# Optimization experiments

Hardware: AMD Instinct MI355X
Metric: run time of the kernel (lower is better)

Reference implementation:

```python
import jax, jax.numpy as jnp
import numpy as np

B, N, D = 256, 131072, 256
TEMP = 0.05
EPS_SM = 1e-6
EPS_LOG = 1e-6
NUM_CLUSTERS = 1000


def _l2norm(x):
    return x / jnp.linalg.norm(x, axis=-1, keepdims=True)


def setup_inputs() -> dict:
    key = jax.random.key(0)
    k1, k2, k3, k4, k5 = jax.random.split(key, 5)
    # re-ID features are L2-normalized in practice; keeps exp(logits/temp) finite
    inputs = _l2norm(jax.random.normal(k1, (B, D), jnp.float32))
    indexes = jax.random.randint(k2, (B,), 0, N)
    labels = jax.random.randint(k3, (N,), 0, NUM_CLUSTERS)  # pseudo cluster ids buffer
    cluster_features = _l2norm(jax.random.normal(k4, (N, D), jnp.float32))
    instance_features = _l2norm(jax.random.normal(k5, (N, D), jnp.float32))
    return {
        "inputs": inputs,
        "cluster_features": cluster_features,
        "instance_features": instance_features,
        "indexes": indexes,
        "labels": labels,
    }


def reference(inputs, cluster_features, instance_features, indexes, labels):
    # targets = labels[indexes]
    targets = labels[indexes]
    # bank similarity GEMM, temperature scaling
    logits = jnp.matmul(inputs, cluster_features.T) / TEMP  # [B, N]
    # module's custom softmax: exp / (sum + eps)  (intentionally no max-subtract)
    exps = jnp.exp(logits)
    masked_sim = exps / (jnp.sum(exps, axis=1, keepdims=True) + EPS_SM)
    logp = jnp.log(masked_sim + EPS_LOG)
    # F.nll_loss: mean of -logp at target column
    loss = -jnp.mean(jnp.take_along_axis(logp, targets[:, None], axis=1))
    return loss
```

## Files before the change

### kernel.cpp

```cpp
#include <hip/hip_runtime.h>
#include <hip/hip_bf16.h>
#include <cstdint>

#define B_ 256
#define N_ 131072
#define D_ 256
#define INV_TEMP 20.0f
#define EPS_SM 1e-6f
#define EPS_LOG 1e-6f

#define TPB 512
#define BROWS 256
#define BN 32
#define BK 64
#define NCHUNK 32
#define LDB 72
#define BUFE (BN * LDB)
#define NSLOT 32
#define NBLK (N_ / BROWS)

typedef __bf16 bf16_t;
typedef bf16_t bf16x8 __attribute__((ext_vector_type(8)));
typedef float f32x4 __attribute__((ext_vector_type(4)));

__device__ inline ushort f2bf(float f) {
  uint32_t u = __builtin_bit_cast(uint32_t, f);
  u += 0x7FFFu + ((u >> 16) & 1u);
  return (ushort)(u >> 16);
}

__global__ __launch_bounds__(TPB, 4)
void gemm_rowsum_fused(const float* __restrict__ inp, const float* __restrict__ cf,
                       const int* __restrict__ idx, const int* __restrict__ lab,
                       float* __restrict__ rowsum, unsigned* __restrict__ counter,
                       float* __restrict__ out) {
  __shared__ ushort smem[B_ * LDB];
  __shared__ unsigned done;
  const int tid  = threadIdx.x;
  const int wave = tid >> 6;
  const int lane = tid & 63;
  const int m15  = lane & 15;
  const int q    = lane >> 4;

  const size_t nbase = (size_t)blockIdx.x * BROWS;
  const int brow = tid >> 4, bcg = tid & 15;
#define LDADDR(c) (cf + (nbase + (size_t)((c) >> 2) * BN + brow) * D_ + ((c) & 3) * BK + bcg * 4)

  float4 ldbuf[2];
  ldbuf[0] = *(const float4*)LDADDR(0);
  ldbuf[1] = *(const float4*)LDADDR(1);

  bf16x8 areg[8][2];
#pragma unroll
  for (int kc = 0; kc < 4; ++kc) {
    const int row = tid >> 1, half = tid & 1;
    const float* src = inp + row * D_ + kc * BK + half * 32;
#pragma unroll
    for (int i = 0; i < 8; ++i) {
      const float4 v = *(const float4*)(src + i * 4);
      ushort4 w = {f2bf(v.x), f2bf(v.y), f2bf(v.z), f2bf(v.w)};
      *(ushort4*)(&smem[row * LDB + half * 32 + i * 4]) = w;
    }
    __syncthreads();
#pragma unroll
    for (int mb = 0; mb < 2; ++mb)
#pragma unroll
      for (int ks = 0; ks < 2; ++ks)
        areg[kc * 2 + ks][mb] = __builtin_bit_cast(
            bf16x8, *(const uint4*)(&smem[(wave * 32 + mb * 16 + m15) * LDB + ks * 32 + q * 8]));
    __syncthreads();
  }

  f32x4 acc[2][2];
  float rs[2][4];
#pragma unroll
  for (int mb = 0; mb < 2; ++mb) {
#pragma unroll
    for (int nb = 0; nb < 2; ++nb) acc[mb][nb] = (f32x4){0.f, 0.f, 0.f, 0.f};
#pragma unroll
    for (int r = 0; r < 4; ++r) rs[mb][r] = 0.f;
  }

  {
    const float4 v = ldbuf[0];
    ushort4 w = {f2bf(v.x), f2bf(v.y), f2bf(v.z), f2bf(v.w)};
    *(ushort4*)(&smem[brow * LDB + bcg * 4]) = w;
  }
  ldbuf[0] = *(const float4*)LDADDR(2);

#pragma unroll
  for (int c = 0; c < NCHUNK; ++c) {
    __syncthreads();
    const ushort* bs = &smem[(c & 1) * BUFE];
#pragma unroll
    for (int ks = 0; ks < 2; ++ks) {
      bf16x8 bfr[2];
#pragma unroll
      for (int nb = 0; nb < 2; ++nb)
        bfr[nb] = __builtin_bit_cast(
            bf16x8, *(const uint4*)(&bs[(nb * 16 + m15) * LDB + ks * 32 + q * 8]));
#pragma unroll
      for (int mb = 0; mb < 2; ++mb)
#pragma unroll
        for (int nb = 0; nb < 2; ++nb)
          acc[mb][nb] = __builtin_amdgcn_mfma_f32_16x16x32_bf16(
              areg[(c & 3) * 2 + ks][mb], bfr[nb], acc[mb][nb], 0, 0, 0);
    }
    if ((c & 3) == 3) {
#pragma unroll
      for (int mb = 0; mb < 2; ++mb)
#pragma unroll
        for (int nb = 0; nb < 2; ++nb)
#pragma unroll
          for (int r = 0; r < 4; ++r)
            rs[mb][r] += __expf(acc[mb][nb][r] * INV_TEMP);
      if (c + 1 < NCHUNK) {
#pragma unroll
        for (int mb = 0; mb < 2; ++mb)
#pragma unroll
          for (int nb = 0; nb < 2; ++nb) acc[mb][nb] = (f32x4){0.f, 0.f, 0.f, 0.f};
      }
    }
    if (c + 1 < NCHUNK) {
      const float4 v = ldbuf[(c + 1) & 1];
      ushort4 w = {f2bf(v.x), f2bf(v.y), f2bf(v.z), f2bf(v.w)};
      *(ushort4*)(&smem[((c + 1) & 1) * BUFE + brow * LDB + bcg * 4]) = w;
    }
    if (c + 3 < NCHUNK) {
      ldbuf[(c + 1) & 1] = *(const float4*)LDADDR(c + 3);
    }
  }

#pragma unroll
  for (int off = 8; off >= 1; off >>= 1)
#pragma unroll
    for (int mb = 0; mb < 2; ++mb)
#pragma unroll
      for (int r = 0; r < 4; ++r)
        rs[mb][r] += __shfl_xor(rs[mb][r], off, 64);

  if (m15 == 0) {
    float* slot = rowsum + (blockIdx.x & (NSLOT - 1)) * B_;
#pragma unroll
    for (int mb = 0; mb < 2; ++mb)
#pragma unroll
      for (int r = 0; r < 4; ++r)
        atomicAdd(&slot[wave * 32 + mb * 16 + q * 4 + r], rs[mb][r]);
  }
#undef LDADDR

  __syncthreads();
  if (tid == 0) {
    __threadfence();
    const unsigned prev = __hip_atomic_fetch_add(counter, 1u, __ATOMIC_ACQ_REL,
                                                 __HIP_MEMORY_SCOPE_AGENT);
    done = (prev == (unsigned)(NBLK - 1)) ? 1u : 0u;
  }
  __syncthreads();
  if (done) {
    __threadfence();
    float* red = (float*)smem;
    const int b = tid >> 1, part = tid & 1;
    const int t = lab[idx[b]];
    const float4* a4 = (const float4*)(inp + b * D_ + part * 128);
    const float4* c4 = (const float4*)(cf + (size_t)t * D_ + part * 128);
    float dot = 0.f;
#pragma unroll
    for (int i = 0; i < 32; ++i) {
      const float4 x = a4[i], y = c4[i];
      dot += x.x * y.x + x.y * y.y + x.z * y.z + x.w * y.w;
    }
    red[tid] = dot;
    __syncthreads();
    if (tid < 256) {
      const float d = red[2 * tid] + red[2 * tid + 1];
      float S = 0.f;
#pragma unroll
      for (int s = 0; s < NSLOT; ++s)
        S += __hip_atomic_load(&rowsum[s * B_ + tid], __ATOMIC_RELAXED,
                               __HIP_MEMORY_SCOPE_AGENT);
      red[512 + tid] = __logf(__expf(d * INV_TEMP) / (S + EPS_SM) + EPS_LOG);
    }
    __syncthreads();
    for (int off = 128; off >= 1; off >>= 1) {
      if (tid < off) red[512 + tid] += red[512 + tid + off];
      __syncthreads();
    }
    if (tid == 0) out[0] = -red[512] * (1.0f / 256.0f);
  }
}

extern "C" void kernel_launch(void* const* d_in, const int* in_sizes, int n_in,
                              void* d_out, int out_size, void* d_ws, size_t ws_size,
                              hipStream_t stream) {
  const float* inp = (const float*)d_in[0];
  const float* cf  = (const float*)d_in[1];
  const int* idx = (const int*)d_in[3];
  const int* lab = (const int*)d_in[4];
  float* out = (float*)d_out;
  float* rowsum = (float*)d_ws;
  unsigned* counter = (unsigned*)(rowsum + NSLOT * B_);

  hipMemsetAsync(d_ws, 0, (NSLOT * B_ + 16) * sizeof(float), stream);
  gemm_rowsum_fused<<<dim3(NBLK), dim3(TPB), 0, stream>>>(inp, cf, idx, lab,
                                                          rowsum, counter, out);
}
```

Measured before the change: 325.1 us.

## Widen N tile to 64, hoist LDS stores before MFMA, use lighter barriers

Doubles the per-chunk N tile from 32 to 64 rows, so each wave issues 8 MFMAs per k-step and there are half as many chunk iterations and barriers. Each thread now loads and converts 8 floats per chunk and writes them with a single 16-byte LDS store. The next buffer's LDS store and global prefetch move ahead of the MFMAs, so conversion overlaps compute. __syncthreads is replaced by a raw lgkmcnt wait plus s_barrier, and f2bf uses the native bf16 cast. This raises register pressure (more accumulators and prefetch registers) at launch bounds 512x4. The single-barrier double-buffer ordering is a correctness hazard: the store into buffer (c+1)&1 right after the barrier targets the buffer other waves read in iteration c-1, which appears safe only because that barrier orders it.

New measurement: 337.1 us. +3.7%, slower.

```diff
diff --git a/kernel.cpp b/kernel.cpp
--- a/kernel.cpp
+++ b/kernel.cpp
@@ -11,9 +11,9 @@
 
 #define TPB 512
 #define BROWS 256
-#define BN 32
+#define BN 64
 #define BK 64
-#define NCHUNK 32
+#define NCHUNK 16
 #define LDB 72
 #define BUFE (BN * LDB)
 #define NSLOT 32
@@ -23,10 +23,22 @@
 typedef bf16_t bf16x8 __attribute__((ext_vector_type(8)));
 typedef float f32x4 __attribute__((ext_vector_type(4)));
 
+struct alignas(16) U8 { ushort u[8]; };
+
 __device__ inline ushort f2bf(float f) {
-  uint32_t u = __builtin_bit_cast(uint32_t, f);
-  u += 0x7FFFu + ((u >> 16) & 1u);
-  return (ushort)(u >> 16);
+  return __builtin_bit_cast(ushort, (__bf16)f);
+}
+
+__device__ inline void cvt_store8(ushort* dst, const float4 a, const float4 b) {
+  U8 w;
+  w.u[0] = f2bf(a.x); w.u[1] = f2bf(a.y); w.u[2] = f2bf(a.z); w.u[3] = f2bf(a.w);
+  w.u[4] = f2bf(b.x); w.u[5] = f2bf(b.y); w.u[6] = f2bf(b.z); w.u[7] = f2bf(b.w);
+  *(uint4*)dst = __builtin_bit_cast(uint4, w);
+}
+
+__device__ inline void bar_ds() {
+  asm volatile("s_waitcnt lgkmcnt(0)" ::: "memory");
+  __builtin_amdgcn_s_barrier();
 }
 
 __global__ __launch_bounds__(TPB, 4)
@@ -43,12 +55,14 @@
   const int q    = lane >> 4;
 
   const size_t nbase = (size_t)blockIdx.x * BROWS;
-  const int brow = tid >> 4, bcg = tid & 15;
-#define LDADDR(c) (cf + (nbase + (size_t)((c) >> 2) * BN + brow) * D_ + ((c) & 3) * BK + bcg * 4)
-
-  float4 ldbuf[2];
-  ldbuf[0] = *(const float4*)LDADDR(0);
-  ldbuf[1] = *(const float4*)LDADDR(1);
+  const int brow = tid >> 3, bcg = tid & 7;
+#define LDADDR(c) (cf + (nbase + (size_t)((c) >> 2) * BN + brow) * D_ + ((c) & 3) * BK + bcg * 8)
+
+  float4 ldbuf[2][2];
+  ldbuf[0][0] = *(const float4*)(LDADDR(0));
+  ldbuf[0][1] = *(const float4*)(LDADDR(0) + 4);
+  ldbuf[1][0] = *(const float4*)(LDADDR(1));
+  ldbuf[1][1] = *(const float4*)(LDADDR(1) + 4);
 
   bf16x8 areg[8][2];
 #pragma unroll
@@ -56,53 +70,58 @@
     const int row = tid >> 1, half = tid & 1;
     const float* src = inp + row * D_ + kc * BK + half * 32;
 #pragma unroll
-    for (int i = 0; i < 8; ++i) {
-      const float4 v = *(const float4*)(src + i * 4);
-      ushort4 w = {f2bf(v.x), f2bf(v.y), f2bf(v.z), f2bf(v.w)};
-      *(ushort4*)(&smem[row * LDB + half * 32 + i * 4]) = w;
-    }
-    __syncthreads();
+    for (int j = 0; j < 4; ++j) {
+      const float4 v0 = *(const float4*)(src + j * 8);
+      const float4 v1 = *(const float4*)(src + j * 8 + 4);
+      cvt_store8(&smem[row * LDB + half * 32 + j * 8], v0, v1);
+    }
+    bar_ds();
 #pragma unroll
     for (int mb = 0; mb < 2; ++mb)
 #pragma unroll
       for (int ks = 0; ks < 2; ++ks)
         areg[kc * 2 + ks][mb] = __builtin_bit_cast(
             bf16x8, *(const uint4*)(&smem[(wave * 32 + mb * 16 + m15) * LDB + ks * 32 + q * 8]));
-    __syncthreads();
-  }
-
-  f32x4 acc[2][2];
+    bar_ds();
+  }
+
+  f32x4 acc[2][4];
   float rs[2][4];
 #pragma unroll
   for (int mb = 0; mb < 2; ++mb) {
 #pragma unroll
-    for (int nb = 0; nb < 2; ++nb) acc[mb][nb] = (f32x4){0.f, 0.f, 0.f, 0.f};
+    for (int nb = 0; nb < 4; ++nb) acc[mb][nb] = (f32x4){0.f, 0.f, 0.f, 0.f};
 #pragma unroll
     for (int r = 0; r < 4; ++r) rs[mb][r] = 0.f;
   }
 
-  {
-    const float4 v = ldbuf[0];
-    ushort4 w = {f2bf(v.x), f2bf(v.y), f2bf(v.z), f2bf(v.w)};
-    *(ushort4*)(&smem[brow * LDB + bcg * 4]) = w;
-  }
-  ldbuf[0] = *(const float4*)LDADDR(2);
+  cvt_store8(&smem[brow * LDB + bcg * 8], ldbuf[0][0], ldbuf[0][1]);
+  ldbuf[0][0] = *(const float4*)(LDADDR(2));
+  ldbuf[0][1] = *(const float4*)(LDADDR(2) + 4);
 
 #pragma unroll
   for (int c = 0; c < NCHUNK; ++c) {
-    __syncthreads();
+    bar_ds();
+    if (c + 1 < NCHUNK) {
+      cvt_store8(&smem[((c + 1) & 1) * BUFE + brow * LDB + bcg * 8],
+                 ldbuf[(c + 1) & 1][0], ldbuf[(c + 1) & 1][1]);
+    }
+    if (c + 3 < NCHUNK) {
+      ldbuf[(c + 1) & 1][0] = *(const float4*)(LDADDR(c + 3));
+      ldbuf[(c + 1) & 1][1] = *(const float4*)(LDADDR(c + 3) + 4);
+    }
     const ushort* bs = &smem[(c & 1) * BUFE];
 #pragma unroll
     for (int ks = 0; ks < 2; ++ks) {
-      bf16x8 bfr[2];
-#pragma unroll
-      for (int nb = 0; nb < 2; ++nb)
+      bf16x8 bfr[4];
+#pragma unroll
+      for (int nb = 0; nb < 4; ++nb)
         bfr[nb] = __builtin_bit_cast(
             bf16x8, *(const uint4*)(&bs[(nb * 16 + m15) * LDB + ks * 32 + q * 8]));
 #pragma unroll
       for (int mb = 0; mb < 2; ++mb)
 #pragma unroll
-        for (int nb = 0; nb < 2; ++nb)
+        for (int nb = 0; nb < 4; ++nb)
           acc[mb][nb] = __builtin_amdgcn_mfma_f32_16x16x32_bf16(
               areg[(c & 3) * 2 + ks][mb], bfr[nb], acc[mb][nb], 0, 0, 0);
     }
@@ -110,7 +129,7 @@
 #pragma unroll
       for (int mb = 0; mb < 2; ++mb)
 #pragma unroll
-        for (int nb = 0; nb < 2; ++nb)
+        for (int nb = 0; nb < 4; ++nb)
 #pragma unroll
           for (int r = 0; r < 4; ++r)
             rs[mb][r] += __expf(acc[mb][nb][r] * INV_TEMP);
@@ -118,16 +137,8 @@
 #pragma unroll
         for (int mb = 0; mb < 2; ++mb)
 #pragma unroll
-          for (int nb = 0; nb < 2; ++nb) acc[mb][nb] = (f32x4){0.f, 0.f, 0.f, 0.f};
+          for (int nb = 0; nb < 4; ++nb) acc[mb][nb] = (f32x4){0.f, 0.f, 0.f, 0.f};
       }
-    }
-    if (c + 1 < NCHUNK) {
-      const float4 v = ldbuf[(c + 1) & 1];
-      ushort4 w = {f2bf(v.x), f2bf(v.y), f2bf(v.z), f2bf(v.w)};
-      *(ushort4*)(&smem[((c + 1) & 1) * BUFE + brow * LDB + bcg * 4]) = w;
-    }
-    if (c + 3 < NCHUNK) {
-      ldbuf[(c + 1) & 1] = *(const float4*)LDADDR(c + 3);
     }
   }
 
```
